# Optimization experiments

Hardware: AMD Instinct MI355X
Metric: run time of the kernel (lower is better)

## Reference

```python
import jax, jax.numpy as jnp
import numpy as np

M1 = M2 = M3 = 8  # retained modes per spatial dim


def get_3d_clifford_kernel(w, g):
    # w: (8, O, I, 2m1, 2m2, 2m3); returns (8O, 8I, 2m1, 2m2, 2m3)
    g0, g1, g2 = g[0], g[1], g[2]
    k0 = jnp.concatenate([w[0], w[1] * g0, w[2] * g1, w[3] * g2, -w[4] * g0 * g1, -w[5] * g0 * g2, -w[6] * g1 * g2, -w[7] * g0 * g1 * g2], axis=1)
    k1 = jnp.concatenate([w[1], w[0], -w[4] * g1, -w[5] * g2, w[2] * g1, w[3] * g2, -w[7] * g1 * g2, -w[6] * g1 * g2], axis=1)
    k2 = jnp.concatenate([w[2], w[4] * g0, w[0], -w[6] * g2, -w[1] * g0, w[7] * g0 * g2, w[3] * g2, w[5] * g0 * g2], axis=1)
    k3 = jnp.concatenate([w[3], w[5] * g0, w[6] * g1, w[0], -w[7] * g0 * g1, -w[1] * g0, -w[2] * g1, -w[4] * g0 * g1], axis=1)
    k4 = jnp.concatenate([w[4], w[2], -w[1], g2 * w[7], w[0], -w[6] * g2, w[5] * g2, w[3] * g2], axis=1)
    k5 = jnp.concatenate([w[5], w[3], -w[7] * g1, -w[1], w[6] * g1, w[0], -w[4] * g1, -w[2] * g1], axis=1)
    k6 = jnp.concatenate([w[6], w[7] * g0, w[3], -w[2], -w[5] * g0, w[4] * g0, w[0], w[1] * g0], axis=1)
    k7 = jnp.concatenate([w[7], w[6], -w[5], w[4], w[3], -w[2], w[1], w[0]], axis=1)
    return jnp.concatenate([k0, k1, k2, k3, k4, k5, k6, k7], axis=0)


def setup_inputs() -> dict:
    key = jax.random.key(0)
    k1, k2 = jax.random.split(key)
    B, D, H, W, Cin, Cout = 4, 48, 48, 48, 24, 24
    x = jax.random.normal(k1, (B, D, H, W, Cin, 8), dtype=jnp.float32)
    scale = 1.0 / (Cin * Cout)
    weights = scale * jax.random.uniform(k2, (8, Cout, Cin, 2 * M1, 2 * M2, 2 * M3), dtype=jnp.float32)
    return {"x": x, "weights": weights}


def reference(x, weights):
    B, D, H, W, Cin, _ = x.shape
    Cout = weights.shape[1]
    g = jnp.ones(3, dtype=x.dtype)  # metric (1, 1, 1)
    # complex-dual packing of the 8 blades
    d1 = x[..., 0] + 1j * x[..., 7]
    d2 = x[..., 1] + 1j * x[..., 6]
    d3 = x[..., 2] + 1j * x[..., 5]
    d4 = x[..., 3] + 1j * x[..., 4]
    f1 = jnp.fft.fftn(d1, axes=(1, 2, 3))
    f2 = jnp.fft.fftn(d2, axes=(1, 2, 3))
    f3 = jnp.fft.fftn(d3, axes=(1, 2, 3))
    f4 = jnp.fft.fftn(d4, axes=(1, 2, 3))
    bchw = lambda t: t.transpose(0, 4, 1, 2, 3)
    # (B, 8*Cin, D, H, W) real tensor of blade spectra
    mv_ft = jnp.concatenate([bchw(f1.real), bchw(f2.real), bchw(f3.real), bchw(f4.real),
                             bchw(f4.imag), bchw(f3.imag), bchw(f2.imag), bchw(f1.imag)], axis=1)
    # gather the 8 low/high-frequency octant corners -> (B, 8Cin, 2m1, 2m2, 2m3)
    i1 = jnp.concatenate([jnp.arange(M1), jnp.arange(D - M1, D)])
    i2 = jnp.concatenate([jnp.arange(M2), jnp.arange(H - M2, H)])
    i3 = jnp.concatenate([jnp.arange(M3), jnp.arange(W - M3, W)])
    input_mul = mv_ft[:, :, i1[:, None, None], i2[None, :, None], i3[None, None, :]]
    kernel = get_3d_clifford_kernel(weights, g)  # (8Cout, 8Cin, 2m1, 2m2, 2m3)
    output_mul = jnp.einsum("bixyz,oixyz->boxyz", input_mul, kernel)
    # scatter back to full spectrum
    out_ft = jnp.zeros((B, 8 * Cout, D, H, W), dtype=mv_ft.dtype)
    out_ft = out_ft.at[:, :, i1[:, None, None], i2[None, :, None], i3[None, None, :]].set(output_mul)
    out_ft = out_ft.reshape(B, 8, Cout, D, H, W).transpose(0, 2, 3, 4, 5, 1)  # (B, Cout, D, H, W, 8)
    o1 = out_ft[..., 0] + 1j * out_ft[..., 7]
    o2 = out_ft[..., 1] + 1j * out_ft[..., 6]
    o3 = out_ft[..., 2] + 1j * out_ft[..., 5]
    o4 = out_ft[..., 3] + 1j * out_ft[..., 4]
    g1_ = jnp.fft.ifftn(o1, axes=(2, 3, 4))
    g2_ = jnp.fft.ifftn(o2, axes=(2, 3, 4))
    g3_ = jnp.fft.ifftn(o3, axes=(2, 3, 4))
    g4_ = jnp.fft.ifftn(o4, axes=(2, 3, 4))
    output = jnp.stack([g1_.real, g2_.real, g3_.real, g4_.real,
                        g4_.imag, g3_.imag, g2_.imag, g1_.imag], axis=-1)  # (B, Cout, D, H, W, 8)
    return output.transpose(0, 2, 3, 4, 1, 5)  # (B, D, H, W, Cout, 8)
```

## Files before the change

### kernel.cpp

```cpp
#include <hip/hip_runtime.h>
#include <math.h>


#define C866 0.8660254037844386f

constexpr float FC0[8] = {1.0f, 0.99144486137885f, 0.96592582628907f, 0.92387953251129f,
                          0.86602540378444f, 0.79335334029124f, 0.70710678118655f, 0.60876142900872f};
constexpr float FS0[8] = {0.0f, 0.13052619222005f, 0.25881904510252f, 0.38268343236509f,
                          0.5f, 0.60876142900872f, 0.70710678118655f, 0.79335334029124f};
constexpr float FC1[8] = {0.5f, 0.60876142900872f, 0.70710678118655f, 0.79335334029124f,
                          0.86602540378444f, 0.92387953251129f, 0.96592582628907f, 0.99144486137885f};
constexpr float FS1[8] = {-0.86602540378444f, -0.79335334029124f, -0.70710678118655f, -0.60876142900872f,
                          -0.5f, -0.38268343236509f, -0.25881904510252f, -0.13052619222005f};

constexpr float CS48[48] = {
  1.0f, 0.99144486137885f, 0.96592582628907f, 0.92387953251129f, 0.86602540378444f,
  0.79335334029124f, 0.70710678118655f, 0.60876142900872f, 0.5f, 0.38268343236509f,
  0.25881904510252f, 0.13052619222005f, 0.0f, -0.13052619222005f, -0.25881904510252f,
  -0.38268343236509f, -0.5f, -0.60876142900872f, -0.70710678118655f, -0.79335334029124f,
  -0.86602540378444f, -0.92387953251129f, -0.96592582628907f, -0.99144486137885f, -1.0f,
  -0.99144486137885f, -0.96592582628907f, -0.92387953251129f, -0.86602540378444f,
  -0.79335334029124f, -0.70710678118655f, -0.60876142900872f, -0.5f, -0.38268343236509f,
  -0.25881904510252f, -0.13052619222005f, 0.0f, 0.13052619222005f, 0.25881904510252f,
  0.38268343236509f, 0.5f, 0.60876142900872f, 0.70710678118655f, 0.79335334029124f,
  0.86602540378444f, 0.92387953251129f, 0.96592582628907f, 0.99144486137885f};
constexpr float SN48[48] = {
  0.0f, 0.13052619222005f, 0.25881904510252f, 0.38268343236509f, 0.5f,
  0.60876142900872f, 0.70710678118655f, 0.79335334029124f, 0.86602540378444f,
  0.92387953251129f, 0.96592582628907f, 0.99144486137885f, 1.0f, 0.99144486137885f,
  0.96592582628907f, 0.92387953251129f, 0.86602540378444f, 0.79335334029124f,
  0.70710678118655f, 0.60876142900872f, 0.5f, 0.38268343236509f, 0.25881904510252f,
  0.13052619222005f, 0.0f, -0.13052619222005f, -0.25881904510252f, -0.38268343236509f,
  -0.5f, -0.60876142900872f, -0.70710678118655f, -0.79335334029124f, -0.86602540378444f,
  -0.92387953251129f, -0.96592582628907f, -0.99144486137885f, -1.0f, -0.99144486137885f,
  -0.96592582628907f, -0.92387953251129f, -0.86602540378444f, -0.79335334029124f,
  -0.70710678118655f, -0.60876142900872f, -0.5f, -0.38268343236509f, -0.25881904510252f,
  -0.13052619222005f};

__device__ __forceinline__ uint32_t c2h(float2 z) {
  union { _Float16 h[2]; uint32_t u; } v;
  v.h[0] = (_Float16)z.x; v.h[1] = (_Float16)z.y;
  return v.u;
}
__device__ __forceinline__ float2 h2c(uint32_t u) {
  union { uint32_t u; _Float16 h[2]; } v;
  v.u = u;
  return make_float2((float)v.h[0], (float)v.h[1]);
}

__device__ __forceinline__ float2 cmul(float2 a, float2 b) {
  return make_float2(fmaf(a.x, b.x, -(a.y * b.y)), fmaf(a.x, b.y, a.y * b.x));
}
__device__ __forceinline__ void cfma(float2& acc, float2 a, float2 t) {
  acc.x = fmaf(a.x, t.x, acc.x); acc.x = fmaf(-a.y, t.y, acc.x);
  acc.y = fmaf(a.x, t.y, acc.y); acc.y = fmaf(a.y, t.x, acc.y);
}

struct FwdState {
  float2 acc[8], t[8], stp[8];
  float2 R1, R2;
};

__device__ __forceinline__ void fwd_init(FwdState& st, int half) {
#pragma unroll
  for (int r = 0; r < 8; ++r) {
    st.acc[r] = make_float2(0.f, 0.f);
    st.t[r] = make_float2(1.f, 0.f);
    st.stp[r] = make_float2(half ? FC1[r] : FC0[r],
                            half ? -FS1[r] : -FS0[r]);
  }
  st.R1 = half ? make_float2(-0.5f, -C866) : make_float2(1.f, 0.f);
  st.R2 = half ? make_float2(-0.5f,  C866) : make_float2(1.f, 0.f);
}

__device__ __forceinline__ void fwd_stepf(FwdState& st, float2 z0, float2 z1, float2 z2) {
  z1 = cmul(z1, st.R1);
  z2 = cmul(z2, st.R2);
  const float sx = z1.x + z2.x, sy = z1.y + z2.y;
  const float dx = z1.x - z2.x, dy = z1.y - z2.y;
  const float2 y0 = make_float2(z0.x + sx, z0.y + sy);
  const float tx = fmaf(-0.5f, sx, z0.x), ty = fmaf(-0.5f, sy, z0.y);
  const float ex = C866 * dx, ey = C866 * dy;
  const float2 y1 = make_float2(tx + ey, ty - ex);
  const float2 y2 = make_float2(tx - ey, ty + ex);
#pragma unroll
  for (int r = 0; r < 8; ++r) {
    const float2 yy = (r % 3 == 0) ? y0 : ((r % 3 == 1) ? y1 : y2);
    cfma(st.acc[r], yy, st.t[r]);
    st.t[r] = cmul(st.t[r], st.stp[r]);
  }
}

struct InvState {
  float2 zr[16], t[16];
};

__device__ __forceinline__ void inv_init(InvState& st, int j0) {
#pragma unroll
  for (int m = 0; m < 16; ++m) {
    const int f = (m < 8) ? m : (m + 32);
    const int ph = (f * j0) % 48;
    st.t[m] = make_float2(CS48[ph], SN48[ph]);
  }
}

__device__ __forceinline__ void inv_stepf(InvState& st, float2& o0, float2& o1, float2& o2) {
  constexpr int JG[16] = {0,1,2,0,1,2,0,1, 1,2,0,1,2,0,1,2};
  float2 u0 = make_float2(0.f, 0.f), u1 = u0, u2 = u0;
#pragma unroll
  for (int m = 0; m < 16; ++m) {
    float2& uu = (JG[m] == 0) ? u0 : ((JG[m] == 1) ? u1 : u2);
    cfma(uu, st.zr[m], st.t[m]);
    const float2 stp = (m < 8) ? make_float2(FC0[m], FS0[m])
                               : make_float2(FC1[m - 8], FS1[m - 8]);
    st.t[m] = cmul(st.t[m], stp);
  }
  const float sx = u1.x + u2.x, sy = u1.y + u2.y;
  const float dx = u1.x - u2.x, dy = u1.y - u2.y;
  o0 = make_float2(u0.x + sx, u0.y + sy);
  const float tx = fmaf(-0.5f, sx, u0.x), ty = fmaf(-0.5f, sy, u0.y);
  const float ex = C866 * dx, ey = C866 * dy;
  o1 = make_float2(tx - ey, ty + ex);
  o2 = make_float2(tx + ey, ty - ex);
}

__global__ __launch_bounds__(192) void k_fwd_w(const float* __restrict__ x,
                                               uint32_t* __restrict__ A) {
  const int q = threadIdx.x % 96, half = threadIdx.x / 96;
  const int ci = q >> 2, c = q & 3;
  const float* xp = x + (size_t)blockIdx.x * 9216 + ci * 8;
  const int reo = c, imo = 7 - c;

  FwdState st;
  fwd_init(st, half);
#pragma unroll 4
  for (int j = 0; j < 16; ++j) {
    const float2 z0 = make_float2(xp[j * 192 + reo], xp[j * 192 + imo]);
    const float2 z1 = make_float2(xp[(j + 16) * 192 + reo], xp[(j + 16) * 192 + imo]);
    const float2 z2 = make_float2(xp[(j + 32) * 192 + reo], xp[(j + 32) * 192 + imo]);
    fwd_stepf(st, z0, z1, z2);
  }
  uint32_t* Ap = A + (size_t)blockIdx.x * 1536 + q;
#pragma unroll
  for (int r = 0; r < 8; ++r) Ap[(half * 8 + r) * 96] = c2h(st.acc[r]);
}

__global__ __launch_bounds__(192) void k_fwd_h(const uint32_t* __restrict__ A,
                                               uint32_t* __restrict__ Bv) {
  const int k3 = blockIdx.x & 15, bd = blockIdx.x >> 4;
  const int q = threadIdx.x % 96, half = threadIdx.x / 96;
  const uint32_t* Ap = A + ((size_t)bd * 768 + k3) * 96 + q;
  FwdState st;
  fwd_init(st, half);
#pragma unroll 4
  for (int j = 0; j < 16; ++j) {
    const float2 z0 = h2c(Ap[(size_t)j * 1536]);
    const float2 z1 = h2c(Ap[(size_t)(j + 16) * 1536]);
    const float2 z2 = h2c(Ap[(size_t)(j + 32) * 1536]);
    fwd_stepf(st, z0, z1, z2);
  }
  uint32_t* Bp = Bv + ((size_t)bd * 256 + k3) * 96 + q;
#pragma unroll
  for (int r = 0; r < 8; ++r) Bp[(size_t)(half * 8 + r) * 1536] = c2h(st.acc[r]);
}

__global__ __launch_bounds__(192) void k_fwd_d(const uint32_t* __restrict__ Bv,
                                               uint32_t* __restrict__ Cv) {
  const int k23 = blockIdx.x & 255, b = blockIdx.x >> 8;
  const int q = threadIdx.x % 96, half = threadIdx.x / 96;
  const uint32_t* Bp = Bv + ((size_t)b * 12288 + k23) * 96 + q;
  FwdState st;
  fwd_init(st, half);
#pragma unroll 4
  for (int j = 0; j < 16; ++j) {
    const float2 z0 = h2c(Bp[(size_t)j * 24576]);
    const float2 z1 = h2c(Bp[(size_t)(j + 16) * 24576]);
    const float2 z2 = h2c(Bp[(size_t)(j + 32) * 24576]);
    fwd_stepf(st, z0, z1, z2);
  }
  uint32_t* Cp = Cv + ((size_t)b * 4096 + k23) * 96 + q;
#pragma unroll
  for (int r = 0; r < 8; ++r) Cp[(size_t)(half * 8 + r) * 24576] = c2h(st.acc[r]);
}

__global__ __launch_bounds__(256) void k_einsum(const uint32_t* __restrict__ Cv,
                                                const float* __restrict__ wgt,
                                                uint32_t* __restrict__ OMz) {
  const int mode = blockIdx.x * 64 + (threadIdx.x & 63);
  const int co = blockIdx.y * 4 + (threadIdx.x >> 6);
  const int cih = blockIdx.z;

  constexpr int WIDX[8][8] = {
      {0, 1, 2, 3, 4, 5, 6, 7}, {1, 0, 4, 5, 2, 3, 7, 6},
      {2, 4, 0, 6, 1, 7, 3, 5}, {3, 5, 6, 0, 7, 1, 2, 4},
      {4, 2, 1, 7, 0, 6, 5, 3}, {5, 3, 7, 1, 6, 0, 4, 2},
      {6, 7, 3, 2, 5, 4, 0, 1}, {7, 6, 5, 4, 3, 2, 1, 0}};
  constexpr int SGN[8][8] = {
      {1, 1, 1, 1, -1, -1, -1, -1}, {1, 1, -1, -1, 1, 1, -1, -1},
      {1, 1, 1, -1, -1, 1, 1, 1},   {1, 1, 1, 1, -1, -1, -1, -1},
      {1, 1, -1, 1, 1, -1, 1, 1},   {1, 1, -1, -1, 1, 1, -1, -1},
      {1, 1, 1, -1, -1, 1, 1, 1},   {1, 1, -1, 1, 1, -1, 1, 1}};

  float acc[8][4];
#pragma unroll
  for (int bo = 0; bo < 8; ++bo)
#pragma unroll
    for (int b = 0; b < 4; ++b) acc[bo][b] = 0.f;

#pragma unroll 2
  for (int cc = 0; cc < 12; ++cc) {
    const int ci = cih * 12 + cc;
    float w8[8];
#pragma unroll
    for (int k = 0; k < 8; ++k)
      w8[k] = wgt[(size_t)((k * 24 + co) * 24 + ci) * 4096 + mode];
#pragma unroll
    for (int b = 0; b < 4; ++b) {
      const uint4 U = *(const uint4*)(Cv + ((size_t)(b * 4096 + mode) * 96 + ci * 4));
      const float2 z0 = h2c(U.x), z1 = h2c(U.y), z2 = h2c(U.z), z3 = h2c(U.w);
      const float inv[8] = {z0.x, z1.x, z2.x, z3.x, z3.y, z2.y, z1.y, z0.y};
#pragma unroll
      for (int bo = 0; bo < 8; ++bo) {
#pragma unroll
        for (int bi = 0; bi < 8; ++bi) {
          const float wv = w8[WIDX[bo][bi]];
          if (SGN[bo][bi] > 0)
            acc[bo][b] = fmaf(wv, inv[bi], acc[bo][b]);
          else
            acc[bo][b] = fmaf(wv, -inv[bi], acc[bo][b]);
        }
      }
    }
  }
  uint32_t* OMp = OMz + (size_t)cih * 1572864;
#pragma unroll
  for (int b = 0; b < 4; ++b) {
    uint4 P;
    P.x = c2h(make_float2(acc[0][b], acc[7][b]));
    P.y = c2h(make_float2(acc[1][b], acc[6][b]));
    P.z = c2h(make_float2(acc[2][b], acc[5][b]));
    P.w = c2h(make_float2(acc[3][b], acc[4][b]));
    *(uint4*)(OMp + ((size_t)(b * 4096 + mode) * 96 + co * 4)) = P;
  }
}

__global__ __launch_bounds__(192) void k_inv_d(const uint32_t* __restrict__ OMz,
                                               uint32_t* __restrict__ IS1) {
  const int col = blockIdx.x * 2 + threadIdx.x / 96;
  const int q = threadIdx.x % 96;
  const int k23 = col & 255, b = col >> 8;
  const int j0 = blockIdx.y * 8;
  InvState st;
#pragma unroll
  for (int m = 0; m < 16; ++m) {
    const size_t idx = ((size_t)b * 4096 + m * 256 + k23) * 96 + q;
    const float2 pa = h2c(OMz[idx]);
    const float2 pb = h2c(OMz[idx + 1572864]);
    st.zr[m] = make_float2(pa.x + pb.x, pa.y + pb.y);
  }
  inv_init(st, j0);
  uint32_t* Op = IS1 + ((size_t)b * 12288 + k23) * 96 + q;
#pragma unroll 2
  for (int jj = 0; jj < 8; ++jj) {
    const int j = j0 + jj;
    float2 o0, o1, o2;
    inv_stepf(st, o0, o1, o2);
    Op[(size_t)j * 24576] = c2h(o0);
    Op[(size_t)(j + 16) * 24576] = c2h(o1);
    Op[(size_t)(j + 32) * 24576] = c2h(o2);
  }
}

__global__ __launch_bounds__(192) void k_inv_h(const uint32_t* __restrict__ IS1,
                                               uint32_t* __restrict__ IS2) {
  const int col = blockIdx.x * 2 + threadIdx.x / 96;
  const int q = threadIdx.x % 96;
  const int m3 = col & 15, bd = col >> 4;
  InvState st;
#pragma unroll
  for (int m = 0; m < 16; ++m)
    st.zr[m] = h2c(IS1[((size_t)bd * 256 + m * 16 + m3) * 96 + q]);
  inv_init(st, 0);
  uint32_t* Op = IS2 + ((size_t)bd * 768 + m3) * 96 + q;
#pragma unroll 2
  for (int j = 0; j < 16; ++j) {
    float2 o0, o1, o2;
    inv_stepf(st, o0, o1, o2);
    Op[(size_t)j * 1536] = c2h(o0);
    Op[(size_t)(j + 16) * 1536] = c2h(o1);
    Op[(size_t)(j + 32) * 1536] = c2h(o2);
  }
}

__global__ __launch_bounds__(192) void k_inv_w(const uint32_t* __restrict__ IS2,
                                               float* __restrict__ out) {
  const int blk = blockIdx.x * 2 + threadIdx.x / 96;
  const int q = threadIdx.x % 96;
  const int co = q >> 2, c = q & 3;
  const float norm = 1.0f / 110592.0f;
  InvState st;
#pragma unroll
  for (int m = 0; m < 16; ++m) {
    float2 z = h2c(IS2[((size_t)blk * 16 + m) * 96 + q]);
    st.zr[m] = make_float2(z.x * norm, z.y * norm);
  }
  inv_init(st, 0);
  float* ob = out + (size_t)blk * 9216 + co * 8;
#pragma unroll 2
  for (int j = 0; j < 16; ++j) {
    float2 o0, o1, o2;
    inv_stepf(st, o0, o1, o2);
    float* p0 = ob + (size_t)j * 192;
    float* p1 = ob + (size_t)(j + 16) * 192;
    float* p2 = ob + (size_t)(j + 32) * 192;
    __builtin_nontemporal_store(o0.x, p0 + c);
    __builtin_nontemporal_store(o0.y, p0 + 7 - c);
    __builtin_nontemporal_store(o1.x, p1 + c);
    __builtin_nontemporal_store(o1.y, p1 + 7 - c);
    __builtin_nontemporal_store(o2.x, p2 + c);
    __builtin_nontemporal_store(o2.y, p2 + 7 - c);
  }
}

extern "C" void kernel_launch(void* const* d_in, const int* in_sizes, int n_in,
                              void* d_out, int out_size, void* d_ws, size_t ws_size,
                              hipStream_t stream) {
  (void)in_sizes; (void)n_in; (void)out_size; (void)ws_size;
  const float* x = (const float*)d_in[0];
  const float* wgt = (const float*)d_in[1];
  float* out = (float*)d_out;

  char* ob = (char*)d_out;
  uint32_t* A   = (uint32_t*)(ob + 0);
  uint32_t* Bv  = (uint32_t*)(ob + 56623104);
  uint32_t* Cv  = (uint32_t*)(ob + 75497472);
  uint32_t* OMz = (uint32_t*)(ob + 81788928);
  uint32_t* IS1 = (uint32_t*)(ob + 0);
  uint32_t* IS2 = (uint32_t*)d_ws;

  k_fwd_w<<<9216, 192, 0, stream>>>(x, A);
  k_fwd_h<<<3072, 192, 0, stream>>>(A, Bv);
  k_fwd_d<<<1024, 192, 0, stream>>>(Bv, Cv);
  k_einsum<<<dim3(64, 6, 2), 256, 0, stream>>>(Cv, wgt, OMz);
  k_inv_d<<<dim3(512, 2), 192, 0, stream>>>(OMz, IS1);
  k_inv_h<<<1536, 192, 0, stream>>>(IS1, IS2);
  k_inv_w<<<4608, 192, 0, stream>>>(IS2, out);
}
```

Before: 324.8 us.

## Fuse W/H forward and H/W inverse DFT passes through shared memory

Merges the forward W and H partial-DFT kernels into one block per (b,d) slab that keeps the intermediate spectrum in shared memory, and does the same for the inverse H and W passes. This removes the global round trips for the A and IS2 intermediates. The einsum no longer splits the input channels across blocks and k_inv_d no longer splits its output rows, so the two-partial sum goes away at the cost of less parallelism in those stages. It also drops the non-temporal output stores, and the fused kernels run fewer, larger blocks with about 75 KB of shared memory each, which may limit occupancy.

```diff
diff --git a/kernel.cpp b/kernel.cpp
--- a/kernel.cpp
+++ b/kernel.cpp
@@ -47,7 +47,6 @@
   v.u = u;
   return make_float2((float)v.h[0], (float)v.h[1]);
 }
-
 __device__ __forceinline__ float2 cmul(float2 a, float2 b) {
   return make_float2(fmaf(a.x, b.x, -(a.y * b.y)), fmaf(a.x, b.y, a.y * b.x));
 }
@@ -56,23 +55,46 @@
   acc.y = fmaf(a.x, t.y, acc.y); acc.y = fmaf(a.y, t.x, acc.y);
 }
 
-struct FwdState {
-  float2 acc[8], t[8], stp[8];
-  float2 R1, R2;
-};
+struct FwdF { float2 acc[16], t[16]; };
+
+__device__ __forceinline__ void fwdf_init(FwdF& st) {
+#pragma unroll
+  for (int k = 0; k < 16; ++k) {
+    st.acc[k] = make_float2(0.f, 0.f);
+    st.t[k] = make_float2(1.f, 0.f);
+  }
+}
+__device__ __forceinline__ void fwdf_step(FwdF& st, float2 z0, float2 z1, float2 z2) {
+  const float sx = z1.x + z2.x, sy = z1.y + z2.y;
+  const float dx = z1.x - z2.x, dy = z1.y - z2.y;
+  float2 y[3];
+  y[0] = make_float2(z0.x + sx, z0.y + sy);
+  const float tx = fmaf(-0.5f, sx, z0.x), ty = fmaf(-0.5f, sy, z0.y);
+  const float ex = C866 * dx, ey = C866 * dy;
+  y[1] = make_float2(tx + ey, ty - ex);
+  y[2] = make_float2(tx - ey, ty + ex);
+  constexpr int SEL[16] = {0,1,2,0,1,2,0,1, 1,2,0,1,2,0,1,2};
+#pragma unroll
+  for (int k = 0; k < 16; ++k) {
+    cfma(st.acc[k], y[SEL[k]], st.t[k]);
+    const float2 stp = (k < 8) ? make_float2(FC0[k], -FS0[k])
+                               : make_float2(FC1[k - 8], -FS1[k - 8]);
+    st.t[k] = cmul(st.t[k], stp);
+  }
+}
+
+struct FwdState { float2 acc[8], t[8], stp[8]; float2 R1, R2; };
 
 __device__ __forceinline__ void fwd_init(FwdState& st, int half) {
 #pragma unroll
   for (int r = 0; r < 8; ++r) {
     st.acc[r] = make_float2(0.f, 0.f);
     st.t[r] = make_float2(1.f, 0.f);
-    st.stp[r] = make_float2(half ? FC1[r] : FC0[r],
-                            half ? -FS1[r] : -FS0[r]);
+    st.stp[r] = make_float2(half ? FC1[r] : FC0[r], half ? -FS1[r] : -FS0[r]);
   }
   st.R1 = half ? make_float2(-0.5f, -C866) : make_float2(1.f, 0.f);
   st.R2 = half ? make_float2(-0.5f,  C866) : make_float2(1.f, 0.f);
 }
-
 __device__ __forceinline__ void fwd_stepf(FwdState& st, float2 z0, float2 z1, float2 z2) {
   z1 = cmul(z1, st.R1);
   z2 = cmul(z2, st.R2);
@@ -91,9 +113,7 @@
   }
 }
 
-struct InvState {
-  float2 zr[16], t[16];
-};
+struct InvState { float2 zr[16], t[16]; };
 
 __device__ __forceinline__ void inv_init(InvState& st, int j0) {
 #pragma unroll
@@ -103,7 +123,6 @@
     st.t[m] = make_float2(CS48[ph], SN48[ph]);
   }
 }
-
 __device__ __forceinline__ void inv_stepf(InvState& st, float2& o0, float2& o1, float2& o2) {
   constexpr int JG[16] = {0,1,2,0,1,2,0,1, 1,2,0,1,2,0,1,2};
   float2 u0 = make_float2(0.f, 0.f), u1 = u0, u2 = u0;
@@ -124,44 +143,49 @@
   o2 = make_float2(tx + ey, ty - ex);
 }
 
-__global__ __launch_bounds__(192) void k_fwd_w(const float* __restrict__ x,
-                                               uint32_t* __restrict__ A) {
-  const int q = threadIdx.x % 96, half = threadIdx.x / 96;
+__global__ __launch_bounds__(384) void k_fwd_wh(const float* __restrict__ x,
+                                                uint32_t* __restrict__ Bv) {
+  __shared__ uint32_t sb[48 * 392];
+  const int bd = blockIdx.x, qg = blockIdx.y;
+  const int tid = threadIdx.x;
+  const int ql = tid % 24;
+  const int q = qg * 24 + ql;
   const int ci = q >> 2, c = q & 3;
-  const float* xp = x + (size_t)blockIdx.x * 9216 + ci * 8;
-  const int reo = c, imo = 7 - c;
-
-  FwdState st;
-  fwd_init(st, half);
-#pragma unroll 4
-  for (int j = 0; j < 16; ++j) {
-    const float2 z0 = make_float2(xp[j * 192 + reo], xp[j * 192 + imo]);
-    const float2 z1 = make_float2(xp[(j + 16) * 192 + reo], xp[(j + 16) * 192 + imo]);
-    const float2 z2 = make_float2(xp[(j + 32) * 192 + reo], xp[(j + 32) * 192 + imo]);
-    fwd_stepf(st, z0, z1, z2);
-  }
-  uint32_t* Ap = A + (size_t)blockIdx.x * 1536 + q;
-#pragma unroll
-  for (int r = 0; r < 8; ++r) Ap[(half * 8 + r) * 96] = c2h(st.acc[r]);
-}
-
-__global__ __launch_bounds__(192) void k_fwd_h(const uint32_t* __restrict__ A,
-                                               uint32_t* __restrict__ Bv) {
-  const int k3 = blockIdx.x & 15, bd = blockIdx.x >> 4;
-  const int q = threadIdx.x % 96, half = threadIdx.x / 96;
-  const uint32_t* Ap = A + ((size_t)bd * 768 + k3) * 96 + q;
-  FwdState st;
-  fwd_init(st, half);
-#pragma unroll 4
-  for (int j = 0; j < 16; ++j) {
-    const float2 z0 = h2c(Ap[(size_t)j * 1536]);
-    const float2 z1 = h2c(Ap[(size_t)(j + 16) * 1536]);
-    const float2 z2 = h2c(Ap[(size_t)(j + 32) * 1536]);
-    fwd_stepf(st, z0, z1, z2);
-  }
-  uint32_t* Bp = Bv + ((size_t)bd * 256 + k3) * 96 + q;
-#pragma unroll
-  for (int r = 0; r < 8; ++r) Bp[(size_t)(half * 8 + r) * 1536] = c2h(st.acc[r]);
+
+  {
+    const float* xb = x + (size_t)bd * 442368 + ci * 8;
+    for (int hh = 0; hh < 3; ++hh) {
+      const int h = hh * 16 + tid / 24;
+      const float* xp = xb + (size_t)h * 9216;
+      FwdF st;
+      fwdf_init(st);
+      for (int j = 0; j < 16; ++j) {
+        const float2 z0 = make_float2(xp[j * 192 + c], xp[j * 192 + 7 - c]);
+        const float2 z1 = make_float2(xp[(j + 16) * 192 + c], xp[(j + 16) * 192 + 7 - c]);
+        const float2 z2 = make_float2(xp[(j + 32) * 192 + c], xp[(j + 32) * 192 + 7 - c]);
+        fwdf_step(st, z0, z1, z2);
+      }
+      uint32_t* sp = &sb[h * 392 + ql];
+#pragma unroll
+      for (int kk = 0; kk < 16; ++kk) sp[kk * 24] = c2h(st.acc[kk]);
+    }
+  }
+  __syncthreads();
+  {
+    const int k3 = tid / 24;
+    const uint32_t* sp = &sb[k3 * 24 + ql];
+    FwdF st;
+    fwdf_init(st);
+    for (int j = 0; j < 16; ++j) {
+      const float2 z0 = h2c(sp[j * 392]);
+      const float2 z1 = h2c(sp[(j + 16) * 392]);
+      const float2 z2 = h2c(sp[(j + 32) * 392]);
+      fwdf_step(st, z0, z1, z2);
+    }
+    uint32_t* Bp = Bv + ((size_t)bd * 256 + k3) * 96 + q;
+#pragma unroll
+    for (int kk = 0; kk < 16; ++kk) Bp[(size_t)kk * 1536] = c2h(st.acc[kk]);
+  }
 }
 
 __global__ __launch_bounds__(192) void k_fwd_d(const uint32_t* __restrict__ Bv,
@@ -188,7 +212,6 @@
                                                 uint32_t* __restrict__ OMz) {
   const int mode = blockIdx.x * 64 + (threadIdx.x & 63);
   const int co = blockIdx.y * 4 + (threadIdx.x >> 6);
-  const int cih = blockIdx.z;
 
   constexpr int WIDX[8][8] = {
       {0, 1, 2, 3, 4, 5, 6, 7}, {1, 0, 4, 5, 2, 3, 7, 6},
@@ -207,9 +230,7 @@
 #pragma unroll
     for (int b = 0; b < 4; ++b) acc[bo][b] = 0.f;
 
-#pragma unroll 2
-  for (int cc = 0; cc < 12; ++cc) {
-    const int ci = cih * 12 + cc;
+  for (int ci = 0; ci < 24; ++ci) {
     float w8[8];
 #pragma unroll
     for (int k = 0; k < 8; ++k)
@@ -232,7 +253,6 @@
       }
     }
   }
-  uint32_t* OMp = OMz + (size_t)cih * 1572864;
 #pragma unroll
   for (int b = 0; b < 4; ++b) {
     uint4 P;
@@ -240,7 +260,7 @@
     P.y = c2h(make_float2(acc[1][b], acc[6][b]));
     P.z = c2h(make_float2(acc[2][b], acc[5][b]));
     P.w = c2h(make_float2(acc[3][b], acc[4][b]));
-    *(uint4*)(OMp + ((size_t)(b * 4096 + mode) * 96 + co * 4)) = P;
+    *(uint4*)(OMz + ((size_t)(b * 4096 + mode) * 96 + co * 4)) = P;
   }
 }
 
@@ -249,20 +269,14 @@
   const int col = blockIdx.x * 2 + threadIdx.x / 96;
   const int q = threadIdx.x % 96;
   const int k23 = col & 255, b = col >> 8;
-  const int j0 = blockIdx.y * 8;
   InvState st;
 #pragma unroll
-  for (int m = 0; m < 16; ++m) {
-    const size_t idx = ((size_t)b * 4096 + m * 256 + k23) * 96 + q;
-    const float2 pa = h2c(OMz[idx]);
-    const float2 pb = h2c(OMz[idx + 1572864]);
-    st.zr[m] = make_float2(pa.x + pb.x, pa.y + pb.y);
-  }
-  inv_init(st, j0);
+  for (int m = 0; m < 16; ++m)
+    st.zr[m] = h2c(OMz[((size_t)b * 4096 + m * 256 + k23) * 96 + q]);
+  inv_init(st, 0);
   uint32_t* Op = IS1 + ((size_t)b * 12288 + k23) * 96 + q;
 #pragma unroll 2
-  for (int jj = 0; jj < 8; ++jj) {
-    const int j = j0 + jj;
+  for (int j = 0; j < 16; ++j) {
     float2 o0, o1, o2;
     inv_stepf(st, o0, o1, o2);
     Op[(size_t)j * 24576] = c2h(o0);
@@ -271,54 +285,58 @@
   }
 }
 
-__global__ __launch_bounds__(192) void k_inv_h(const uint32_t* __restrict__ IS1,
-                                               uint32_t* __restrict__ IS2) {
-  const int col = blockIdx.x * 2 + threadIdx.x / 96;
-  const int q = threadIdx.x % 96;
-  const int m3 = col & 15, bd = col >> 4;
-  InvState st;
-#pragma unroll
-  for (int m = 0; m < 16; ++m)
-    st.zr[m] = h2c(IS1[((size_t)bd * 256 + m * 16 + m3) * 96 + q]);
-  inv_init(st, 0);
-  uint32_t* Op = IS2 + ((size_t)bd * 768 + m3) * 96 + q;
+__global__ __launch_bounds__(384) void k_inv_hw(const uint32_t* __restrict__ IS1,
+                                                float* __restrict__ out) {
+  __shared__ uint32_t sb[48 * 392];
+  const int bd = blockIdx.x, qg = blockIdx.y;
+  const int tid = threadIdx.x;
+  const int ql = tid % 24;
+  const int q = qg * 24 + ql;
+
+  {
+    const int m3 = tid / 24;
+    InvState st;
+#pragma unroll
+    for (int m2 = 0; m2 < 16; ++m2)
+      st.zr[m2] = h2c(IS1[((size_t)bd * 256 + m2 * 16 + m3) * 96 + q]);
+    inv_init(st, 0);
+    uint32_t* sp = &sb[m3 * 24 + ql];
 #pragma unroll 2
-  for (int j = 0; j < 16; ++j) {
-    float2 o0, o1, o2;
-    inv_stepf(st, o0, o1, o2);
-    Op[(size_t)j * 1536] = c2h(o0);
-    Op[(size_t)(j + 16) * 1536] = c2h(o1);
-    Op[(size_t)(j + 32) * 1536] = c2h(o2);
-  }
-}
-
-__global__ __launch_bounds__(192) void k_inv_w(const uint32_t* __restrict__ IS2,
-                                               float* __restrict__ out) {
-  const int blk = blockIdx.x * 2 + threadIdx.x / 96;
-  const int q = threadIdx.x % 96;
-  const int co = q >> 2, c = q & 3;
-  const float norm = 1.0f / 110592.0f;
-  InvState st;
-#pragma unroll
-  for (int m = 0; m < 16; ++m) {
-    float2 z = h2c(IS2[((size_t)blk * 16 + m) * 96 + q]);
-    st.zr[m] = make_float2(z.x * norm, z.y * norm);
-  }
-  inv_init(st, 0);
-  float* ob = out + (size_t)blk * 9216 + co * 8;
+    for (int j = 0; j < 16; ++j) {
+      float2 o0, o1, o2;
+      inv_stepf(st, o0, o1, o2);
+      sp[(size_t)j * 392] = c2h(o0);
+      sp[(size_t)(j + 16) * 392] = c2h(o1);
+      sp[(size_t)(j + 32) * 392] = c2h(o2);
+    }
+  }
+  __syncthreads();
+  {
+    const int co = q >> 2, c = q & 3;
+    const float norm = 1.0f / 110592.0f;
+    for (int hh = 0; hh < 3; ++hh) {
+      const int h = hh * 16 + tid / 24;
+      const uint32_t* sp = &sb[h * 392 + ql];
+      InvState st;
+#pragma unroll
+      for (int m3 = 0; m3 < 16; ++m3) {
+        const float2 z = h2c(sp[m3 * 24]);
+        st.zr[m3] = make_float2(z.x * norm, z.y * norm);
+      }
+      inv_init(st, 0);
+      float* ob = out + (((size_t)bd * 48 + h) * 48) * 192 + co * 8;
 #pragma unroll 2
-  for (int j = 0; j < 16; ++j) {
-    float2 o0, o1, o2;
-    inv_stepf(st, o0, o1, o2);
-    float* p0 = ob + (size_t)j * 192;
-    float* p1 = ob + (size_t)(j + 16) * 192;
-    float* p2 = ob + (size_t)(j + 32) * 192;
-    __builtin_nontemporal_store(o0.x, p0 + c);
-    __builtin_nontemporal_store(o0.y, p0 + 7 - c);
-    __builtin_nontemporal_store(o1.x, p1 + c);
-    __builtin_nontemporal_store(o1.y, p1 + 7 - c);
-    __builtin_nontemporal_store(o2.x, p2 + c);
-    __builtin_nontemporal_store(o2.y, p2 + 7 - c);
+      for (int j = 0; j < 16; ++j) {
+        float2 o0, o1, o2;
+        inv_stepf(st, o0, o1, o2);
+        float* p0 = ob + (size_t)j * 192;
+        float* p1 = ob + (size_t)(j + 16) * 192;
+        float* p2 = ob + (size_t)(j + 32) * 192;
+        p0[c] = o0.x; p0[7 - c] = o0.y;
+        p1[c] = o1.x; p1[7 - c] = o1.y;
+        p2[c] = o2.x; p2[7 - c] = o2.y;
+      }
+    }
   }
 }
 
@@ -331,18 +349,14 @@
   float* out = (float*)d_out;
 
   char* ob = (char*)d_out;
-  uint32_t* A   = (uint32_t*)(ob + 0);
-  uint32_t* Bv  = (uint32_t*)(ob + 56623104);
-  uint32_t* Cv  = (uint32_t*)(ob + 75497472);
-  uint32_t* OMz = (uint32_t*)(ob + 81788928);
-  uint32_t* IS1 = (uint32_t*)(ob + 0);
-  uint32_t* IS2 = (uint32_t*)d_ws;
-
-  k_fwd_w<<<9216, 192, 0, stream>>>(x, A);
-  k_fwd_h<<<3072, 192, 0, stream>>>(A, Bv);
+  uint32_t* Bv  = (uint32_t*)(ob + 0);
+  uint32_t* Cv  = (uint32_t*)(ob + 18874368);
+  uint32_t* OMz = (uint32_t*)(ob + 25165824);
+  uint32_t* IS1 = (uint32_t*)d_ws;
+
+  k_fwd_wh<<<dim3(192, 4), 384, 0, stream>>>(x, Bv);
   k_fwd_d<<<1024, 192, 0, stream>>>(Bv, Cv);
-  k_einsum<<<dim3(64, 6, 2), 256, 0, stream>>>(Cv, wgt, OMz);
-  k_inv_d<<<dim3(512, 2), 192, 0, stream>>>(OMz, IS1);
-  k_inv_h<<<1536, 192, 0, stream>>>(IS1, IS2);
-  k_inv_w<<<4608, 192, 0, stream>>>(IS2, out);
-}
+  k_einsum<<<dim3(64, 6), 256, 0, stream>>>(Cv, wgt, OMz);
+  k_inv_d<<<512, 192, 0, stream>>>(OMz, IS1);
+  k_inv_hw<<<dim3(192, 4), 384, 0, stream>>>(IS1, out);
+}
```

Result: slower. 346.2 us (+6.6%).
